# Kernel optimization log

Hardware: AMD Instinct MI355X
Metric: run time of the kernel (lower is better)

Reference implementation:

```python
import jax, jax.numpy as jnp
import numpy as np

BN_EPS = 1e-5


def setup_inputs() -> dict:
    key = jax.random.key(0)
    k1, k2, k3, k4, k5 = jax.random.split(key, 5)
    B, M, N = 4, 65536, 16384
    C_pre, C_cur, D_out = 64, 128, 128
    C_in = C_pre + C_cur  # 192
    pre_x = jax.random.normal(k1, (B, C_pre, M), dtype=jnp.float32)
    cur_x = jax.random.normal(k2, (B, C_cur, N), dtype=jnp.float32)
    up_idx = jax.random.randint(k3, (B, M, 1), 0, N, dtype=jnp.int64)
    w = jax.random.normal(k4, (C_in, D_out), dtype=jnp.float32) * 0.05
    b = jax.random.normal(k5, (D_out,), dtype=jnp.float32) * 0.05
    gamma = jnp.ones((D_out,), dtype=jnp.float32)
    beta = jnp.zeros((D_out,), dtype=jnp.float32)
    run_mean = jnp.zeros((D_out,), dtype=jnp.float32)
    run_var = jnp.ones((D_out,), dtype=jnp.float32)
    return {"pre_x": pre_x, "cur_x": cur_x, "up_idx": up_idx, "w": w, "b": b,
            "gamma": gamma, "beta": beta, "run_mean": run_mean, "run_var": run_var}


def reference(pre_x, cur_x, up_idx, w, b, gamma, beta, run_mean, run_var):
    # indexing_neighbor(cur_x.permute(0,2,1), up_idx).squeeze(2):
    # gather coarse-point features at nearest-neighbor indices -> [B, C_cur, M]
    idx = up_idx[:, :, 0]                                   # [B, M]
    feat = jnp.take_along_axis(cur_x, idx[:, None, :], axis=2)  # [B, C_cur, M]
    x = jnp.concatenate([pre_x, feat], axis=1)              # [B, C_in, M]
    # ConvTranspose1d(kernel=1) == pointwise linear with weight [C_in, D_out]
    y = jnp.einsum('bcm,cd->bdm', x, w) + b[None, :, None]  # [B, D_out, M]
    # BatchNorm1d (inference form with running stats) + ReLU
    inv = jax.lax.rsqrt(run_var + BN_EPS)
    y = (y - run_mean[None, :, None]) * (inv * gamma)[None, :, None] + beta[None, :, None]
    y = jnp.maximum(y, 0.0)
    return y.transpose(0, 2, 1)                             # [B, M, D_out]
```

## Files before the change

### kernel.cpp

```cpp
#include <hip/hip_runtime.h>
#include <hip/hip_bf16.h>


typedef short bhalf8 __attribute__((ext_vector_type(8)));
typedef float f32x4 __attribute__((ext_vector_type(4)));
typedef unsigned int u32x4 __attribute__((ext_vector_type(4)));

__device__ __forceinline__ short f2bf(float f) {
  unsigned int u = __float_as_uint(f);
  unsigned int r = (u + 0x7fffu + ((u >> 16) & 1u)) >> 16;
  return (short)r;
}
__device__ __forceinline__ float bf2f(short s) {
  return __uint_as_float(((unsigned int)(unsigned short)s) << 16);
}

#define ZST 136
#define PST 72

__global__ __launch_bounds__(256, 4) void cur_gemm(const float* __restrict__ cur,
                                                   const float* __restrict__ w,
                                                   short* __restrict__ Z) {
  __shared__ short lds[64 * ZST];
  const int tid = threadIdx.x;
  const int lane = tid & 63;
  const int wv = tid >> 6;
  const int c = lane & 15;
  const int g = lane >> 4;
  const int r0 = blockIdx.x << 6;
  const int b = r0 >> 14;
  const int n0 = r0 & 16383;
  const float* src = cur + (size_t)b * 128 * 16384 + n0;

  bhalf8 bw[4][2];
#pragma unroll
  for (int s = 0; s < 4; ++s)
#pragma unroll
    for (int ct = 0; ct < 2; ++ct) {
      const int col = 32 * wv + 16 * ct + c;
#pragma unroll
      for (int j = 0; j < 8; ++j)
        bw[s][ct][j] = f2bf(w[(64 + 32 * s + 8 * g + j) * 128 + col]);
    }

#pragma unroll
  for (int it = 0; it < 8; ++it) {
    int v = it * 256 + tid;
    int cc = v >> 4;
    int nq = (v & 15) << 2;
    f32x4 f = __builtin_nontemporal_load(
        reinterpret_cast<const f32x4*>(&src[(size_t)cc * 16384 + nq]));
#pragma unroll
    for (int k = 0; k < 4; ++k) lds[(nq + k) * ZST + cc] = f2bf(f[k]);
  }
  __syncthreads();

  f32x4 acc[4][2];
#pragma unroll
  for (int rt = 0; rt < 4; ++rt) {
    bhalf8 a[4];
#pragma unroll
    for (int s = 0; s < 4; ++s)
      a[s] = *reinterpret_cast<const bhalf8*>(&lds[(16 * rt + c) * ZST + 32 * s + 8 * g]);
    acc[rt][0] = (f32x4){0.f, 0.f, 0.f, 0.f};
    acc[rt][1] = (f32x4){0.f, 0.f, 0.f, 0.f};
#pragma unroll
    for (int s = 0; s < 4; ++s) {
      acc[rt][0] = __builtin_amdgcn_mfma_f32_16x16x32_bf16(a[s], bw[s][0], acc[rt][0], 0, 0, 0);
      acc[rt][1] = __builtin_amdgcn_mfma_f32_16x16x32_bf16(a[s], bw[s][1], acc[rt][1], 0, 0, 0);
    }
  }
  __syncthreads();
#pragma unroll
  for (int rt = 0; rt < 4; ++rt)
#pragma unroll
    for (int ct = 0; ct < 2; ++ct)
#pragma unroll
      for (int i = 0; i < 4; ++i)
        lds[(16 * rt + 4 * g + i) * ZST + 32 * wv + 16 * ct + c] = f2bf(acc[rt][ct][i]);
  __syncthreads();
  short* dst = Z + (size_t)r0 * 128;
  const int row = tid >> 2, q = tid & 3;
#pragma unroll
  for (int u = 0; u < 4; ++u) {
    bhalf8 pk = *reinterpret_cast<const bhalf8*>(&lds[row * ZST + q * 32 + 8 * u]);
    __builtin_nontemporal_store(pk, reinterpret_cast<bhalf8*>(&dst[(size_t)row * 128 + q * 32 + 8 * u]));
  }
}

#define NBLK 2048

__global__ __launch_bounds__(256, 4) void fused_main(
    const float* __restrict__ pre_x,
    const int* __restrict__ up_idx,
    const float* __restrict__ w,
    const float* __restrict__ bias, const float* __restrict__ gamma,
    const float* __restrict__ beta, const float* __restrict__ rmean,
    const float* __restrict__ rvar,
    const short* __restrict__ Z,
    float* __restrict__ out)
{
  __shared__ short pre_lds[64 * PST];
  __shared__ short z_lds[64 * ZST];
  const int tid = threadIdx.x;
  const int lane = tid & 63;
  const int wv = tid >> 6;
  const int c = lane & 15;
  const int g = lane >> 4;

  bhalf8 bw[2][2];
#pragma unroll
  for (int s = 0; s < 2; ++s)
#pragma unroll
    for (int ct = 0; ct < 2; ++ct) {
      const int col = 32 * wv + 16 * ct + c;
#pragma unroll
      for (int j = 0; j < 8; ++j)
        bw[s][ct][j] = f2bf(w[(32 * s + 8 * g + j) * 128 + col]);
    }
  float scale[2], shift[2];
#pragma unroll
  for (int ct = 0; ct < 2; ++ct) {
    const int d = 32 * wv + 16 * ct + c;
    float sc = gamma[d] * rsqrtf(rvar[d] + 1e-5f);
    scale[ct] = sc;
    shift[ct] = (bias[d] - rmean[d]) * sc + beta[d];
  }

  for (int t = 0; t < 2; ++t) {
    const long rg = blockIdx.x + (long)t * NBLK;
    const long r0 = rg << 6;
    const int b = (int)(r0 >> 16);
    const int m0 = (int)(r0 & 65535);
    if (t) __syncthreads();

    {
      const float* pb = pre_x + (size_t)b * 64 * 65536 + m0;
#pragma unroll
      for (int it = 0; it < 4; ++it) {
        int v = it * 256 + tid;
        int cc = v >> 4;
        int mq = (v & 15) << 2;
        f32x4 f = __builtin_nontemporal_load(
            reinterpret_cast<const f32x4*>(&pb[(size_t)cc * 65536 + mq]));
#pragma unroll
        for (int k = 0; k < 4; ++k) pre_lds[(mq + k) * PST + cc] = f2bf(f[k]);
      }
    }
    {
#pragma unroll
      for (int it = 0; it < 4; ++it) {
        int mm = it * 16 + (tid >> 4);
        int seg = tid & 15;
        int n = up_idx[r0 + mm];
        const short* srcp = Z + ((size_t)b * 16384 + n) * 128 + seg * 8;
        *reinterpret_cast<u32x4*>(&z_lds[mm * ZST + seg * 8]) =
            *reinterpret_cast<const u32x4*>(srcp);
      }
    }
    __syncthreads();

#pragma unroll
    for (int rt = 0; rt < 4; ++rt) {
      bhalf8 a[2];
#pragma unroll
      for (int s = 0; s < 2; ++s)
        a[s] = *reinterpret_cast<const bhalf8*>(
            &pre_lds[(16 * rt + c) * PST + 32 * s + 8 * g]);
      f32x4 acc0 = {0.f, 0.f, 0.f, 0.f};
      f32x4 acc1 = {0.f, 0.f, 0.f, 0.f};
#pragma unroll
      for (int s = 0; s < 2; ++s) {
        acc0 = __builtin_amdgcn_mfma_f32_16x16x32_bf16(a[s], bw[s][0], acc0, 0, 0, 0);
        acc1 = __builtin_amdgcn_mfma_f32_16x16x32_bf16(a[s], bw[s][1], acc1, 0, 0, 0);
      }
      float* ob = out + (size_t)(r0 + 16 * rt + 4 * g) * 128 + 32 * wv;
#pragma unroll
      for (int i = 0; i < 4; ++i) {
        const short* zr = &z_lds[(16 * rt + 4 * g + i) * ZST + 32 * wv];
        float z0 = bf2f(zr[c]);
        float z1 = bf2f(zr[16 + c]);
        float v0 = fmaxf((acc0[i] + z0) * scale[0] + shift[0], 0.f);
        float v1 = fmaxf((acc1[i] + z1) * scale[1] + shift[1], 0.f);
        __builtin_nontemporal_store(v0, ob + (size_t)i * 128 + c);
        __builtin_nontemporal_store(v1, ob + (size_t)i * 128 + 16 + c);
      }
    }
  }
}

extern "C" void kernel_launch(void* const* d_in, const int* in_sizes, int n_in,
                              void* d_out, int out_size, void* d_ws, size_t ws_size,
                              hipStream_t stream) {
  const float* pre_x = (const float*)d_in[0];
  const float* cur_x = (const float*)d_in[1];
  const int* up_idx = (const int*)d_in[2];
  const float* w = (const float*)d_in[3];
  const float* bias = (const float*)d_in[4];
  const float* gamma = (const float*)d_in[5];
  const float* beta = (const float*)d_in[6];
  const float* rmean = (const float*)d_in[7];
  const float* rvar = (const float*)d_in[8];
  float* out = (float*)d_out;
  short* Z = (short*)d_ws;

  hipLaunchKernelGGL(cur_gemm, dim3(1024), dim3(256), 0, stream, cur_x, w, Z);
  hipLaunchKernelGGL(fused_main, dim3(NBLK), dim3(256), 0, stream, pre_x, up_idx, w,
                     bias, gamma, beta, rmean, rvar, Z, out);
}
```

Measured before the change: 248.2 us.

## Merge both stages into one cooperative persistent kernel with grid sync

Replaces the two launches (coarse-point GEMM, then gather plus fine GEMM) with a single cooperative kernel of 1024 persistent blocks that runs phase 1, does a grid-wide sync, then runs phase 2. Tiles shrink from 64 to 32 rows so each block loops over several tiles, and a two-kernel fallback is used if the cooperative launch fails. The aim is to remove the inter-kernel launch gap and tail effects. The cost is a grid barrier, smaller tiles that reuse weight registers less per barrier, and Z stores that are no longer nontemporal.

```diff
diff --git a/kernel.cpp b/kernel.cpp
--- a/kernel.cpp
+++ b/kernel.cpp
@@ -1,6 +1,9 @@
 #include <hip/hip_runtime.h>
 #include <hip/hip_bf16.h>
-
+#include <hip/hip_cooperative_groups.h>
+
+
+namespace cg = cooperative_groups;
 
 typedef short bhalf8 __attribute__((ext_vector_type(8)));
 typedef float f32x4 __attribute__((ext_vector_type(4)));
@@ -17,20 +20,17 @@
 
 #define ZST 136
 #define PST 72
-
-__global__ __launch_bounds__(256, 4) void cur_gemm(const float* __restrict__ cur,
-                                                   const float* __restrict__ w,
-                                                   short* __restrict__ Z) {
-  __shared__ short lds[64 * ZST];
+#define SMEM_SHORTS (32 * ZST + 32 * PST)
+
+__device__ __forceinline__ void run_phase1(int bx, int nb, int tiles,
+                                           const float* __restrict__ cur_x,
+                                           const float* __restrict__ w,
+                                           short* Z, short* tile_lds) {
   const int tid = threadIdx.x;
   const int lane = tid & 63;
   const int wv = tid >> 6;
   const int c = lane & 15;
   const int g = lane >> 4;
-  const int r0 = blockIdx.x << 6;
-  const int b = r0 >> 14;
-  const int n0 = r0 & 16383;
-  const float* src = cur + (size_t)b * 128 * 16384 + n0;
 
   bhalf8 bw[4][2];
 #pragma unroll
@@ -43,65 +43,68 @@
         bw[s][ct][j] = f2bf(w[(64 + 32 * s + 8 * g + j) * 128 + col]);
     }
 
-#pragma unroll
-  for (int it = 0; it < 8; ++it) {
-    int v = it * 256 + tid;
-    int cc = v >> 4;
-    int nq = (v & 15) << 2;
-    f32x4 f = __builtin_nontemporal_load(
-        reinterpret_cast<const f32x4*>(&src[(size_t)cc * 16384 + nq]));
-#pragma unroll
-    for (int k = 0; k < 4; ++k) lds[(nq + k) * ZST + cc] = f2bf(f[k]);
-  }
-  __syncthreads();
-
-  f32x4 acc[4][2];
-#pragma unroll
-  for (int rt = 0; rt < 4; ++rt) {
-    bhalf8 a[4];
-#pragma unroll
-    for (int s = 0; s < 4; ++s)
-      a[s] = *reinterpret_cast<const bhalf8*>(&lds[(16 * rt + c) * ZST + 32 * s + 8 * g]);
-    acc[rt][0] = (f32x4){0.f, 0.f, 0.f, 0.f};
-    acc[rt][1] = (f32x4){0.f, 0.f, 0.f, 0.f};
-#pragma unroll
-    for (int s = 0; s < 4; ++s) {
-      acc[rt][0] = __builtin_amdgcn_mfma_f32_16x16x32_bf16(a[s], bw[s][0], acc[rt][0], 0, 0, 0);
-      acc[rt][1] = __builtin_amdgcn_mfma_f32_16x16x32_bf16(a[s], bw[s][1], acc[rt][1], 0, 0, 0);
-    }
-  }
-  __syncthreads();
-#pragma unroll
-  for (int rt = 0; rt < 4; ++rt)
-#pragma unroll
-    for (int ct = 0; ct < 2; ++ct)
-#pragma unroll
-      for (int i = 0; i < 4; ++i)
-        lds[(16 * rt + 4 * g + i) * ZST + 32 * wv + 16 * ct + c] = f2bf(acc[rt][ct][i]);
-  __syncthreads();
-  short* dst = Z + (size_t)r0 * 128;
-  const int row = tid >> 2, q = tid & 3;
-#pragma unroll
-  for (int u = 0; u < 4; ++u) {
-    bhalf8 pk = *reinterpret_cast<const bhalf8*>(&lds[row * ZST + q * 32 + 8 * u]);
-    __builtin_nontemporal_store(pk, reinterpret_cast<bhalf8*>(&dst[(size_t)row * 128 + q * 32 + 8 * u]));
-  }
-}
-
-#define NBLK 2048
-
-__global__ __launch_bounds__(256, 4) void fused_main(
-    const float* __restrict__ pre_x,
-    const int* __restrict__ up_idx,
-    const float* __restrict__ w,
-    const float* __restrict__ bias, const float* __restrict__ gamma,
-    const float* __restrict__ beta, const float* __restrict__ rmean,
-    const float* __restrict__ rvar,
-    const short* __restrict__ Z,
-    float* __restrict__ out)
-{
-  __shared__ short pre_lds[64 * PST];
-  __shared__ short z_lds[64 * ZST];
+  for (int t = 0; t < tiles; ++t) {
+    const int r0 = (bx + t * nb) << 5;
+    const int b = r0 >> 14;
+    const int n0 = r0 & 16383;
+    const float* src = cur_x + (size_t)b * 128 * 16384 + n0;
+    if (t) __syncthreads();
+#pragma unroll
+    for (int it = 0; it < 4; ++it) {
+      int v = it * 256 + tid;
+      int cc = v >> 3;
+      int nq = (v & 7) << 2;
+      f32x4 f = __builtin_nontemporal_load(
+          reinterpret_cast<const f32x4*>(&src[(size_t)cc * 16384 + nq]));
+#pragma unroll
+      for (int k = 0; k < 4; ++k) tile_lds[(nq + k) * ZST + cc] = f2bf(f[k]);
+    }
+    __syncthreads();
+    f32x4 acc[2][2];
+#pragma unroll
+    for (int rt = 0; rt < 2; ++rt) {
+      bhalf8 a[4];
+#pragma unroll
+      for (int s = 0; s < 4; ++s)
+        a[s] = *reinterpret_cast<const bhalf8*>(&tile_lds[(16 * rt + c) * ZST + 32 * s + 8 * g]);
+      acc[rt][0] = (f32x4){0.f, 0.f, 0.f, 0.f};
+      acc[rt][1] = (f32x4){0.f, 0.f, 0.f, 0.f};
+#pragma unroll
+      for (int s = 0; s < 4; ++s) {
+        acc[rt][0] = __builtin_amdgcn_mfma_f32_16x16x32_bf16(a[s], bw[s][0], acc[rt][0], 0, 0, 0);
+        acc[rt][1] = __builtin_amdgcn_mfma_f32_16x16x32_bf16(a[s], bw[s][1], acc[rt][1], 0, 0, 0);
+      }
+    }
+    __syncthreads();
+#pragma unroll
+    for (int rt = 0; rt < 2; ++rt)
+#pragma unroll
+      for (int ct = 0; ct < 2; ++ct)
+#pragma unroll
+        for (int i = 0; i < 4; ++i)
+          tile_lds[(16 * rt + 4 * g + i) * ZST + 32 * wv + 16 * ct + c] = f2bf(acc[rt][ct][i]);
+    __syncthreads();
+    short* dst = Z + (size_t)r0 * 128;
+    const int row = tid >> 3, q = tid & 7;
+#pragma unroll
+    for (int u = 0; u < 2; ++u) {
+      bhalf8 pk = *reinterpret_cast<const bhalf8*>(&tile_lds[row * ZST + q * 16 + 8 * u]);
+      *reinterpret_cast<bhalf8*>(&dst[(size_t)row * 128 + q * 16 + 8 * u]) = pk;
+    }
+  }
+}
+
+__device__ __forceinline__ void run_phase2(int bx, int nb, int tiles,
+                                           const float* __restrict__ pre_x,
+                                           const int* __restrict__ up_idx,
+                                           const float* __restrict__ w,
+                                           const float* __restrict__ bias,
+                                           const float* __restrict__ gamma,
+                                           const float* __restrict__ beta,
+                                           const float* __restrict__ rmean,
+                                           const float* __restrict__ rvar,
+                                           const short* Z, float* __restrict__ out,
+                                           short* z_lds, short* pre_lds) {
   const int tid = threadIdx.x;
   const int lane = tid & 63;
   const int wv = tid >> 6;
@@ -127,46 +130,40 @@
     shift[ct] = (bias[d] - rmean[d]) * sc + beta[d];
   }
 
-  for (int t = 0; t < 2; ++t) {
-    const long rg = blockIdx.x + (long)t * NBLK;
-    const long r0 = rg << 6;
+  for (int t = 0; t < tiles; ++t) {
+    const long rg = bx + (long)t * nb;
+    const long r0 = rg << 5;
     const int b = (int)(r0 >> 16);
     const int m0 = (int)(r0 & 65535);
-    if (t) __syncthreads();
-
+    __syncthreads();
     {
       const float* pb = pre_x + (size_t)b * 64 * 65536 + m0;
 #pragma unroll
-      for (int it = 0; it < 4; ++it) {
+      for (int it = 0; it < 2; ++it) {
         int v = it * 256 + tid;
-        int cc = v >> 4;
-        int mq = (v & 15) << 2;
+        int cc = v >> 3;
+        int mq = (v & 7) << 2;
         f32x4 f = __builtin_nontemporal_load(
             reinterpret_cast<const f32x4*>(&pb[(size_t)cc * 65536 + mq]));
 #pragma unroll
         for (int k = 0; k < 4; ++k) pre_lds[(mq + k) * PST + cc] = f2bf(f[k]);
       }
     }
-    {
-#pragma unroll
-      for (int it = 0; it < 4; ++it) {
-        int mm = it * 16 + (tid >> 4);
-        int seg = tid & 15;
-        int n = up_idx[r0 + mm];
-        const short* srcp = Z + ((size_t)b * 16384 + n) * 128 + seg * 8;
-        *reinterpret_cast<u32x4*>(&z_lds[mm * ZST + seg * 8]) =
-            *reinterpret_cast<const u32x4*>(srcp);
-      }
-    }
-    __syncthreads();
-
-#pragma unroll
-    for (int rt = 0; rt < 4; ++rt) {
+#pragma unroll
+    for (int it = 0; it < 2; ++it) {
+      int mm = it * 16 + (tid >> 4);
+      int seg = tid & 15;
+      int n = up_idx[r0 + mm];
+      *reinterpret_cast<u32x4*>(&z_lds[mm * ZST + seg * 8]) =
+          *reinterpret_cast<const u32x4*>(Z + ((size_t)b * 16384 + n) * 128 + seg * 8);
+    }
+    __syncthreads();
+#pragma unroll
+    for (int rt = 0; rt < 2; ++rt) {
       bhalf8 a[2];
 #pragma unroll
       for (int s = 0; s < 2; ++s)
-        a[s] = *reinterpret_cast<const bhalf8*>(
-            &pre_lds[(16 * rt + c) * PST + 32 * s + 8 * g]);
+        a[s] = *reinterpret_cast<const bhalf8*>(&pre_lds[(16 * rt + c) * PST + 32 * s + 8 * g]);
       f32x4 acc0 = {0.f, 0.f, 0.f, 0.f};
       f32x4 acc1 = {0.f, 0.f, 0.f, 0.f};
 #pragma unroll
@@ -178,15 +175,44 @@
 #pragma unroll
       for (int i = 0; i < 4; ++i) {
         const short* zr = &z_lds[(16 * rt + 4 * g + i) * ZST + 32 * wv];
-        float z0 = bf2f(zr[c]);
-        float z1 = bf2f(zr[16 + c]);
-        float v0 = fmaxf((acc0[i] + z0) * scale[0] + shift[0], 0.f);
-        float v1 = fmaxf((acc1[i] + z1) * scale[1] + shift[1], 0.f);
+        float v0 = fmaxf((acc0[i] + bf2f(zr[c])) * scale[0] + shift[0], 0.f);
+        float v1 = fmaxf((acc1[i] + bf2f(zr[16 + c])) * scale[1] + shift[1], 0.f);
         __builtin_nontemporal_store(v0, ob + (size_t)i * 128 + c);
         __builtin_nontemporal_store(v1, ob + (size_t)i * 128 + 16 + c);
       }
     }
   }
+}
+
+__global__ __launch_bounds__(256, 4) void fused_all(
+    const float* __restrict__ pre_x, const float* __restrict__ cur_x,
+    const int* __restrict__ up_idx, const float* __restrict__ w,
+    const float* __restrict__ bias, const float* __restrict__ gamma,
+    const float* __restrict__ beta, const float* __restrict__ rmean,
+    const float* __restrict__ rvar, short* Z, float* __restrict__ out) {
+  __shared__ short smem[SMEM_SHORTS];
+  run_phase1(blockIdx.x, 1024, 2, cur_x, w, Z, smem);
+  __threadfence();
+  cg::this_grid().sync();
+  run_phase2(blockIdx.x, 1024, 8, pre_x, up_idx, w, bias, gamma, beta, rmean, rvar,
+             Z, out, smem, smem + 32 * ZST);
+}
+
+__global__ __launch_bounds__(256, 4) void k_phase1(const float* __restrict__ cur_x,
+                                                   const float* __restrict__ w,
+                                                   short* Z) {
+  __shared__ short smem[32 * ZST];
+  run_phase1(blockIdx.x, 2048, 1, cur_x, w, Z, smem);
+}
+__global__ __launch_bounds__(256, 4) void k_phase2(
+    const float* __restrict__ pre_x, const int* __restrict__ up_idx,
+    const float* __restrict__ w, const float* __restrict__ bias,
+    const float* __restrict__ gamma, const float* __restrict__ beta,
+    const float* __restrict__ rmean, const float* __restrict__ rvar,
+    const short* Z, float* __restrict__ out) {
+  __shared__ short smem[SMEM_SHORTS];
+  run_phase2(blockIdx.x, 2048, 4, pre_x, up_idx, w, bias, gamma, beta, rmean, rvar,
+             Z, out, smem, smem + 32 * ZST);
 }
 
 extern "C" void kernel_launch(void* const* d_in, const int* in_sizes, int n_in,
@@ -204,7 +230,13 @@
   float* out = (float*)d_out;
   short* Z = (short*)d_ws;
 
-  hipLaunchKernelGGL(cur_gemm, dim3(1024), dim3(256), 0, stream, cur_x, w, Z);
-  hipLaunchKernelGGL(fused_main, dim3(NBLK), dim3(256), 0, stream, pre_x, up_idx, w,
-                     bias, gamma, beta, rmean, rvar, Z, out);
-}
+  void* args[11] = {&pre_x, &cur_x, &up_idx, &w,  &bias, &gamma,
+                    &beta,  &rmean, &rvar,   &Z,  &out};
+  hipError_t e = hipLaunchCooperativeKernel(fused_all, dim3(1024), dim3(256), args,
+                                            0u, stream);
+  if (e != hipSuccess) {
+    hipLaunchKernelGGL(k_phase1, dim3(2048), dim3(256), 0, stream, cur_x, w, Z);
+    hipLaunchKernelGGL(k_phase2, dim3(2048), dim3(256), 0, stream, pre_x, up_idx, w,
+                       bias, gamma, beta, rmean, rvar, Z, out);
+  }
+}
```

Result: slower. 515.6 us (+107.7%).

## Batch global loads into registers before LDS writes and use one tile per block

Applied to the files above, without the earlier changes.

Both kernels now issue all their global loads (cur_x tiles, pre_x tiles, gathered Z rows) into registers before any conversion or LDS store, so more memory requests are in flight at once. fused_main drops its two-tile loop in favour of one 64-row tile per block with a 4096-block grid, and the index and Z gathers are issued ahead of the weight setup. The launch_bounds occupancy hint is removed and Z is written with normal rather than nontemporal stores, which may leave it in cache for the gather. Holding more registers per thread may reduce occupancy.

```diff
diff --git a/kernel.cpp b/kernel.cpp
--- a/kernel.cpp
+++ b/kernel.cpp
@@ -18,9 +18,9 @@
 #define ZST 136
 #define PST 72
 
-__global__ __launch_bounds__(256, 4) void cur_gemm(const float* __restrict__ cur,
-                                                   const float* __restrict__ w,
-                                                   short* __restrict__ Z) {
+__global__ __launch_bounds__(256) void cur_gemm(const float* __restrict__ cur,
+                                                const float* __restrict__ w,
+                                                short* __restrict__ Z) {
   __shared__ short lds[64 * ZST];
   const int tid = threadIdx.x;
   const int lane = tid & 63;
@@ -43,15 +43,20 @@
         bw[s][ct][j] = f2bf(w[(64 + 32 * s + 8 * g + j) * 128 + col]);
     }
 
+  f32x4 cf[8];
+#pragma unroll
+  for (int it = 0; it < 8; ++it) {
+    int v = it * 256 + tid;
+    cf[it] = __builtin_nontemporal_load(
+        reinterpret_cast<const f32x4*>(&src[(size_t)(v >> 4) * 16384 + ((v & 15) << 2)]));
+  }
 #pragma unroll
   for (int it = 0; it < 8; ++it) {
     int v = it * 256 + tid;
     int cc = v >> 4;
     int nq = (v & 15) << 2;
-    f32x4 f = __builtin_nontemporal_load(
-        reinterpret_cast<const f32x4*>(&src[(size_t)cc * 16384 + nq]));
-#pragma unroll
-    for (int k = 0; k < 4; ++k) lds[(nq + k) * ZST + cc] = f2bf(f[k]);
+#pragma unroll
+    for (int k = 0; k < 4; ++k) lds[(nq + k) * ZST + cc] = f2bf(cf[it][k]);
   }
   __syncthreads();
 
@@ -82,15 +87,12 @@
   short* dst = Z + (size_t)r0 * 128;
   const int row = tid >> 2, q = tid & 3;
 #pragma unroll
-  for (int u = 0; u < 4; ++u) {
-    bhalf8 pk = *reinterpret_cast<const bhalf8*>(&lds[row * ZST + q * 32 + 8 * u]);
-    __builtin_nontemporal_store(pk, reinterpret_cast<bhalf8*>(&dst[(size_t)row * 128 + q * 32 + 8 * u]));
-  }
-}
-
-#define NBLK 2048
-
-__global__ __launch_bounds__(256, 4) void fused_main(
+  for (int u = 0; u < 4; ++u)
+    *reinterpret_cast<bhalf8*>(&dst[(size_t)row * 128 + q * 32 + 8 * u]) =
+        *reinterpret_cast<const bhalf8*>(&lds[row * ZST + q * 32 + 8 * u]);
+}
+
+__global__ __launch_bounds__(256) void fused_main(
     const float* __restrict__ pre_x,
     const int* __restrict__ up_idx,
     const float* __restrict__ w,
@@ -107,6 +109,26 @@
   const int wv = tid >> 6;
   const int c = lane & 15;
   const int g = lane >> 4;
+  const int r0 = blockIdx.x << 6;
+  const int b = r0 >> 16;
+  const int m0 = r0 & 65535;
+
+  int ns[4];
+#pragma unroll
+  for (int it = 0; it < 4; ++it) ns[it] = up_idx[r0 + it * 16 + (tid >> 4)];
+  const float* pb = pre_x + (size_t)b * 64 * 65536 + m0;
+  f32x4 pf[4];
+#pragma unroll
+  for (int it = 0; it < 4; ++it) {
+    int v = it * 256 + tid;
+    pf[it] = __builtin_nontemporal_load(
+        reinterpret_cast<const f32x4*>(&pb[(size_t)(v >> 4) * 65536 + ((v & 15) << 2)]));
+  }
+  u32x4 zf[4];
+#pragma unroll
+  for (int it = 0; it < 4; ++it)
+    zf[it] = *reinterpret_cast<const u32x4*>(
+        Z + ((size_t)b * 16384 + ns[it]) * 128 + (tid & 15) * 8);
 
   bhalf8 bw[2][2];
 #pragma unroll
@@ -127,64 +149,42 @@
     shift[ct] = (bias[d] - rmean[d]) * sc + beta[d];
   }
 
-  for (int t = 0; t < 2; ++t) {
-    const long rg = blockIdx.x + (long)t * NBLK;
-    const long r0 = rg << 6;
-    const int b = (int)(r0 >> 16);
-    const int m0 = (int)(r0 & 65535);
-    if (t) __syncthreads();
-
-    {
-      const float* pb = pre_x + (size_t)b * 64 * 65536 + m0;
-#pragma unroll
-      for (int it = 0; it < 4; ++it) {
-        int v = it * 256 + tid;
-        int cc = v >> 4;
-        int mq = (v & 15) << 2;
-        f32x4 f = __builtin_nontemporal_load(
-            reinterpret_cast<const f32x4*>(&pb[(size_t)cc * 65536 + mq]));
-#pragma unroll
-        for (int k = 0; k < 4; ++k) pre_lds[(mq + k) * PST + cc] = f2bf(f[k]);
-      }
-    }
-    {
-#pragma unroll
-      for (int it = 0; it < 4; ++it) {
-        int mm = it * 16 + (tid >> 4);
-        int seg = tid & 15;
-        int n = up_idx[r0 + mm];
-        const short* srcp = Z + ((size_t)b * 16384 + n) * 128 + seg * 8;
-        *reinterpret_cast<u32x4*>(&z_lds[mm * ZST + seg * 8]) =
-            *reinterpret_cast<const u32x4*>(srcp);
-      }
-    }
-    __syncthreads();
-
-#pragma unroll
-    for (int rt = 0; rt < 4; ++rt) {
-      bhalf8 a[2];
-#pragma unroll
-      for (int s = 0; s < 2; ++s)
-        a[s] = *reinterpret_cast<const bhalf8*>(
-            &pre_lds[(16 * rt + c) * PST + 32 * s + 8 * g]);
-      f32x4 acc0 = {0.f, 0.f, 0.f, 0.f};
-      f32x4 acc1 = {0.f, 0.f, 0.f, 0.f};
-#pragma unroll
-      for (int s = 0; s < 2; ++s) {
-        acc0 = __builtin_amdgcn_mfma_f32_16x16x32_bf16(a[s], bw[s][0], acc0, 0, 0, 0);
-        acc1 = __builtin_amdgcn_mfma_f32_16x16x32_bf16(a[s], bw[s][1], acc1, 0, 0, 0);
-      }
-      float* ob = out + (size_t)(r0 + 16 * rt + 4 * g) * 128 + 32 * wv;
-#pragma unroll
-      for (int i = 0; i < 4; ++i) {
-        const short* zr = &z_lds[(16 * rt + 4 * g + i) * ZST + 32 * wv];
-        float z0 = bf2f(zr[c]);
-        float z1 = bf2f(zr[16 + c]);
-        float v0 = fmaxf((acc0[i] + z0) * scale[0] + shift[0], 0.f);
-        float v1 = fmaxf((acc1[i] + z1) * scale[1] + shift[1], 0.f);
-        __builtin_nontemporal_store(v0, ob + (size_t)i * 128 + c);
-        __builtin_nontemporal_store(v1, ob + (size_t)i * 128 + 16 + c);
-      }
+#pragma unroll
+  for (int it = 0; it < 4; ++it) {
+    int v = it * 256 + tid;
+    int cc = v >> 4;
+    int mq = (v & 15) << 2;
+#pragma unroll
+    for (int k = 0; k < 4; ++k) pre_lds[(mq + k) * PST + cc] = f2bf(pf[it][k]);
+  }
+#pragma unroll
+  for (int it = 0; it < 4; ++it)
+    *reinterpret_cast<u32x4*>(&z_lds[(it * 16 + (tid >> 4)) * ZST + (tid & 15) * 8]) =
+        zf[it];
+  __syncthreads();
+
+#pragma unroll
+  for (int rt = 0; rt < 4; ++rt) {
+    bhalf8 a[2];
+#pragma unroll
+    for (int s = 0; s < 2; ++s)
+      a[s] = *reinterpret_cast<const bhalf8*>(
+          &pre_lds[(16 * rt + c) * PST + 32 * s + 8 * g]);
+    f32x4 acc0 = {0.f, 0.f, 0.f, 0.f};
+    f32x4 acc1 = {0.f, 0.f, 0.f, 0.f};
+#pragma unroll
+    for (int s = 0; s < 2; ++s) {
+      acc0 = __builtin_amdgcn_mfma_f32_16x16x32_bf16(a[s], bw[s][0], acc0, 0, 0, 0);
+      acc1 = __builtin_amdgcn_mfma_f32_16x16x32_bf16(a[s], bw[s][1], acc1, 0, 0, 0);
+    }
+    float* ob = out + (size_t)(r0 + 16 * rt + 4 * g) * 128 + 32 * wv;
+#pragma unroll
+    for (int i = 0; i < 4; ++i) {
+      const short* zr = &z_lds[(16 * rt + 4 * g + i) * ZST + 32 * wv];
+      float v0 = fmaxf((acc0[i] + bf2f(zr[c])) * scale[0] + shift[0], 0.f);
+      float v1 = fmaxf((acc1[i] + bf2f(zr[16 + c])) * scale[1] + shift[1], 0.f);
+      __builtin_nontemporal_store(v0, ob + (size_t)i * 128 + c);
+      __builtin_nontemporal_store(v1, ob + (size_t)i * 128 + 16 + c);
     }
   }
 }
@@ -205,6 +205,6 @@
   short* Z = (short*)d_ws;
 
   hipLaunchKernelGGL(cur_gemm, dim3(1024), dim3(256), 0, stream, cur_x, w, Z);
-  hipLaunchKernelGGL(fused_main, dim3(NBLK), dim3(256), 0, stream, pre_x, up_idx, w,
+  hipLaunchKernelGGL(fused_main, dim3(4096), dim3(256), 0, stream, pre_x, up_idx, w,
                      bias, gamma, beta, rmean, rvar, Z, out);
 }
```

Measured after the change: 246.6 us. No clear change (-0.7%).
